# Kernel optimization log

Hardware: AMD Instinct MI355X
Metric: run time of the kernel (lower is better)

The kernel has to match this reference:

```python
import jax, jax.numpy as jnp
import numpy as np

BN_EPS = 1e-5
SEQ_LEN = 256
LSTM_IN = 32
HIDDEN = 512


def setup_inputs() -> dict:
    key = jax.random.key(0)
    ks = jax.random.split(key, 8)
    B, IN_DIM, OUT_DIM = 2048, SEQ_LEN * LSTM_IN, 1
    s_in = 1.0 / np.sqrt(IN_DIM)
    s_h = 1.0 / np.sqrt(HIDDEN)
    return {
        "x": jax.random.normal(ks[0], (B, IN_DIM), jnp.float32),
        "bn_gamma": jnp.ones((IN_DIM,), jnp.float32),
        "bn_beta": jnp.zeros((IN_DIM,), jnp.float32),
        "W_in": jax.random.normal(ks[1], (IN_DIM, IN_DIM), jnp.float32) * s_in,
        "b_in": jax.random.normal(ks[2], (IN_DIM,), jnp.float32) * s_in,
        "W_ih": jax.random.normal(ks[3], (4 * HIDDEN, LSTM_IN), jnp.float32) * s_h,
        "W_hh": jax.random.normal(ks[4], (4 * HIDDEN, HIDDEN), jnp.float32) * s_h,
        "b_ih": jax.random.normal(ks[5], (4 * HIDDEN,), jnp.float32) * s_h,
        "b_hh": jax.random.normal(ks[6], (4 * HIDDEN,), jnp.float32) * s_h,
        "W_out": jax.random.normal(ks[7], (1, HIDDEN), jnp.float32) * s_h,
    }


def reference(x, bn_gamma, bn_beta, W_in, b_in, W_ih, W_hh, b_ih, b_hh, W_out):
    B = x.shape[0]
    # BatchNorm1d (training mode: biased batch statistics)
    mean = jnp.mean(x, axis=0)
    var = jnp.mean((x - mean) ** 2, axis=0)
    out = (x - mean) * jax.lax.rsqrt(var + BN_EPS) * bn_gamma + bn_beta
    # layer_in: Linear(in_dim, in_dim)
    out = out @ W_in.T + b_in
    # split contiguous feature axis into timesteps: [B, T*D] -> [T, B, D]
    xs = out.reshape(B, SEQ_LEN, LSTM_IN).transpose(1, 0, 2)
    # precompute input-to-hidden gates for all steps: [T, B, 4H]
    gates_x = jnp.einsum('tbd,gd->tbg', xs, W_ih) + b_ih + b_hh

    def step(carry, gx):
        h, c = carry
        gates = gx + h @ W_hh.T
        i, f, g, o = jnp.split(gates, 4, axis=-1)
        i = jax.nn.sigmoid(i)
        f = jax.nn.sigmoid(f)
        g = jnp.tanh(g)
        o = jax.nn.sigmoid(o)
        c = f * c + i * g
        h = o * jnp.tanh(c)
        return (h, c), None

    h0 = jnp.zeros((B, HIDDEN), x.dtype)
    c0 = jnp.zeros((B, HIDDEN), x.dtype)
    (h_t, _), _ = jax.lax.scan(step, (h0, c0), gates_x)
    # layer_out: Linear(hidden, out_dim, bias=False)
    return h_t @ W_out.T
```

## Files before the change

### kernel.cpp

```cpp
#include <hip/hip_runtime.h>

#define SEQ   256
#define DIN   8192
#define BATCH 2048
#define HID   512
#define G4    2048
#define KG    544

typedef __attribute__((ext_vector_type(8))) short short8;
typedef __attribute__((ext_vector_type(4))) float f32x4;

static __device__ __forceinline__ unsigned short f2bf(float f) {
  unsigned int u = __float_as_uint(f);
  return (unsigned short)((u + 0x7FFFu + ((u >> 16) & 1u)) >> 16);
}
static __device__ __forceinline__ float bf2f(unsigned short u) {
  return __uint_as_float(((unsigned int)u) << 16);
}
static __device__ __forceinline__ float sigmoidf_(float x) {
  return 1.f / (1.f + __expf(-x));
}
static __device__ __forceinline__ float tanhf_(float x) {
  return 1.f - 2.f / (__expf(2.f * x) + 1.f);
}

__global__ __launch_bounds__(256) void bn_partial(const float* __restrict__ x,
                                                  float* __restrict__ psum,
                                                  float* __restrict__ psq) {
  int c = blockIdx.x * 256 + threadIdx.x;
  int r0 = blockIdx.y * 256;
  float s = 0.f, q = 0.f;
#pragma unroll 8
  for (int r = r0; r < r0 + 256; ++r) {
    float v = x[(size_t)r * DIN + c];
    s += v; q += v * v;
  }
  psum[blockIdx.y * DIN + c] = s;
  psq[blockIdx.y * DIN + c] = q;
}

__global__ __launch_bounds__(256) void bn_finalize(const float* __restrict__ psum,
                                                   const float* __restrict__ psq,
                                                   const float* __restrict__ gamma,
                                                   const float* __restrict__ beta,
                                                   float* __restrict__ scale,
                                                   float* __restrict__ shift) {
  int c = blockIdx.x * 256 + threadIdx.x;
  float s = 0.f, q = 0.f;
#pragma unroll
  for (int i = 0; i < 8; ++i) { s += psum[i * DIN + c]; q += psq[i * DIN + c]; }
  float mean = s * (1.f / BATCH);
  float var = q * (1.f / BATCH) - mean * mean;
  float sc = gamma[c] * rsqrtf(var + 1e-5f);
  scale[c] = sc;
  shift[c] = beta[c] - mean * sc;
}

__global__ __launch_bounds__(256) void cvt_bf16(const float* __restrict__ in,
                                                unsigned short* __restrict__ out, long n) {
  long i = ((long)blockIdx.x * 256 + threadIdx.x) * 8;
  if (i >= n) return;
  float4 a = *(const float4*)(in + i);
  float4 b = *(const float4*)(in + i + 4);
  ushort4 lo, hi;
  lo.x = f2bf(a.x); lo.y = f2bf(a.y); lo.z = f2bf(a.z); lo.w = f2bf(a.w);
  hi.x = f2bf(b.x); hi.y = f2bf(b.y); hi.z = f2bf(b.z); hi.w = f2bf(b.w);
  *(ushort4*)(out + i) = lo;
  *(ushort4*)(out + i + 4) = hi;
}

__global__ __launch_bounds__(256) void build_wg2(const float* __restrict__ W_hh,
                                                 const float* __restrict__ W_ih,
                                                 const float* __restrict__ b_ih,
                                                 const float* __restrict__ b_hh,
                                                 unsigned short* __restrict__ Wg2,
                                                 float* __restrict__ bias2) {
  int gp = blockIdx.x;
  int u = gp >> 2, gate = gp & 3;
  int g = gate * HID + u;
  for (int k = threadIdx.x; k < KG; k += 256) {
    float v = (k < HID) ? W_hh[(size_t)g * HID + k] : W_ih[(size_t)g * 32 + (k - HID)];
    Wg2[(size_t)gp * KG + k] = f2bf(v);
  }
  if (threadIdx.x == 0) bias2[gp] = b_ih[g] + b_hh[g];
}

template<int BF16B>
__global__ __launch_bounds__(256) void gemm1(const float* __restrict__ x,
                                             const float* __restrict__ scale,
                                             const float* __restrict__ shift,
                                             const void* __restrict__ Bsrc,
                                             const float* __restrict__ b_in,
                                             unsigned short* __restrict__ xs) {
  __shared__ unsigned short As[128 * 40];
  __shared__ unsigned short Bs[128 * 40];
  const int tid = threadIdx.x;
  const int lane = tid & 63;
  const int wave = tid >> 6;
  const int wm = (wave >> 1) * 64, wn = (wave & 1) * 64;
  const int bn = blockIdx.x * 128, bm = blockIdx.y * 128;
  const int lr = lane & 15;
  const int kq = (lane >> 4) * 8;

  f32x4 acc[4][4] = {};

  for (int k0 = 0; k0 < DIN; k0 += 32) {
#pragma unroll
    for (int i = 0; i < 4; ++i) {
      int idx = tid + i * 256;
      int row = idx >> 3, c4 = (idx & 7) * 4;
      float4 v = *(const float4*)&x[(size_t)(bm + row) * DIN + k0 + c4];
      float4 sc = *(const float4*)&scale[k0 + c4];
      float4 sh = *(const float4*)&shift[k0 + c4];
      ushort4 o;
      o.x = f2bf(v.x * sc.x + sh.x);
      o.y = f2bf(v.y * sc.y + sh.y);
      o.z = f2bf(v.z * sc.z + sh.z);
      o.w = f2bf(v.w * sc.w + sh.w);
      *(ushort4*)&As[row * 40 + c4] = o;
    }
    if constexpr (BF16B) {
      const unsigned short* W = (const unsigned short*)Bsrc;
#pragma unroll
      for (int i = 0; i < 2; ++i) {
        int idx = tid + i * 256;
        int row = idx >> 2, cc = (idx & 3) * 8;
        *(int4*)&Bs[row * 40 + cc] = *(const int4*)&W[(size_t)(bn + row) * DIN + k0 + cc];
      }
    } else {
      const float* W = (const float*)Bsrc;
#pragma unroll
      for (int i = 0; i < 4; ++i) {
        int idx = tid + i * 256;
        int row = idx >> 3, c4 = (idx & 7) * 4;
        float4 v = *(const float4*)&W[(size_t)(bn + row) * DIN + k0 + c4];
        ushort4 o;
        o.x = f2bf(v.x); o.y = f2bf(v.y); o.z = f2bf(v.z); o.w = f2bf(v.w);
        *(ushort4*)&Bs[row * 40 + c4] = o;
      }
    }
    __syncthreads();
    short8 af[4], bfr[4];
#pragma unroll
    for (int i = 0; i < 4; ++i) af[i] = *(const short8*)&As[(wm + i * 16 + lr) * 40 + kq];
#pragma unroll
    for (int j = 0; j < 4; ++j) bfr[j] = *(const short8*)&Bs[(wn + j * 16 + lr) * 40 + kq];
#pragma unroll
    for (int i = 0; i < 4; ++i)
#pragma unroll
      for (int j = 0; j < 4; ++j)
        acc[i][j] = __builtin_amdgcn_mfma_f32_16x16x32_bf16(af[i], bfr[j], acc[i][j], 0, 0, 0);
    __syncthreads();
  }
#pragma unroll
  for (int i = 0; i < 4; ++i)
#pragma unroll
    for (int j = 0; j < 4; ++j)
#pragma unroll
      for (int r = 0; r < 4; ++r) {
        int row = bm + wm + i * 16 + (lane >> 4) * 4 + r;
        int col = bn + wn + j * 16 + lr;
        float val = acc[i][j][r] + b_in[col];
        xs[((size_t)(col >> 5) * BATCH + row) * 32 + (col & 31)] = f2bf(val);
      }
}

__global__ __launch_bounds__(256) void step_fused(const unsigned short* __restrict__ hin,
                                                  const unsigned short* __restrict__ xst,
                                                  const unsigned short* __restrict__ Wg2,
                                                  const float* __restrict__ bias2,
                                                  float* __restrict__ c,
                                                  unsigned short* __restrict__ hout) {
  __shared__ unsigned short As[64 * 40];
  __shared__ unsigned short Bs[64 * 40];
  __shared__ float gt[64 * 68];
  const int tid = threadIdx.x;
  const int lane = tid & 63;
  const int wave = tid >> 6;
  const int wm = (wave >> 1) * 32, wn = (wave & 1) * 32;
  const int orig = blockIdx.x;
  const int wgid = (orig & 7) * 128 + (orig >> 3);
  const int bx = wgid & 31, by = wgid >> 5;
  const int bm = by * 64, bn = bx * 64;
  const int lr = lane & 15;
  const int kq = (lane >> 4) * 8;
  const int srow = tid >> 2, scc = (tid & 3) * 8;

  f32x4 acc[2][2] = {};

  for (int kt = 0; kt < 17; ++kt) {
    const int k0 = kt * 32;
    int4 av, bv;
    if (kt < 16) av = *(const int4*)&hin[(size_t)(bm + srow) * HID + k0 + scc];
    else         av = *(const int4*)&xst[(size_t)(bm + srow) * 32 + scc];
    bv = *(const int4*)&Wg2[(size_t)(bn + srow) * KG + k0 + scc];
    *(int4*)&As[srow * 40 + scc] = av;
    *(int4*)&Bs[srow * 40 + scc] = bv;
    __syncthreads();
    short8 af[2], bfr[2];
#pragma unroll
    for (int i = 0; i < 2; ++i) af[i] = *(const short8*)&As[(wm + i * 16 + lr) * 40 + kq];
#pragma unroll
    for (int j = 0; j < 2; ++j) bfr[j] = *(const short8*)&Bs[(wn + j * 16 + lr) * 40 + kq];
#pragma unroll
    for (int i = 0; i < 2; ++i)
#pragma unroll
      for (int j = 0; j < 2; ++j)
        acc[i][j] = __builtin_amdgcn_mfma_f32_16x16x32_bf16(af[i], bfr[j], acc[i][j], 0, 0, 0);
    __syncthreads();
  }

#pragma unroll
  for (int i = 0; i < 2; ++i)
#pragma unroll
    for (int j = 0; j < 2; ++j) {
      int colb = wn + j * 16 + lr;
      float bsum = bias2[bn + colb];
#pragma unroll
      for (int r = 0; r < 4; ++r) {
        int row = wm + i * 16 + (lane >> 4) * 4 + r;
        gt[row * 68 + colb] = acc[i][j][r] + bsum;
      }
    }
  __syncthreads();

  {
    const int row = tid >> 2, q = tid & 3;
    const int b = bm + row;
    const int u0 = (bn >> 2) + q * 4;
    const float* gtr = &gt[row * 68 + q * 16];
    const size_t cidx = (size_t)b * HID + u0;
    float4 cold = *(const float4*)&c[cidx];
    float cn[4];
    ushort4 hv;
    const float* co = &cold.x;
#pragma unroll
    for (int k = 0; k < 4; ++k) {
      float iv = sigmoidf_(gtr[k * 4 + 0]);
      float fv = sigmoidf_(gtr[k * 4 + 1]);
      float gv = tanhf_(gtr[k * 4 + 2]);
      float ov = sigmoidf_(gtr[k * 4 + 3]);
      float ccn = fv * co[k] + iv * gv;
      cn[k] = ccn;
      ((unsigned short*)&hv)[k] = f2bf(ov * tanhf_(ccn));
    }
    float4 cw; cw.x = cn[0]; cw.y = cn[1]; cw.z = cn[2]; cw.w = cn[3];
    *(float4*)&c[cidx] = cw;
    *(ushort4*)&hout[cidx] = hv;
  }
}

__global__ __launch_bounds__(64) void gemv_out(const unsigned short* __restrict__ h,
                                               const float* __restrict__ Wout,
                                               float* __restrict__ out) {
  int b = blockIdx.x;
  int lane = threadIdx.x;
  float s = 0.f;
#pragma unroll
  for (int i = 0; i < 8; ++i) {
    int u = lane + i * 64;
    s += bf2f(h[(size_t)b * HID + u]) * Wout[u];
  }
#pragma unroll
  for (int off = 32; off > 0; off >>= 1) s += __shfl_down(s, off);
  if (lane == 0) out[b] = s;
}

extern "C" void kernel_launch(void* const* d_in, const int* in_sizes, int n_in,
                              void* d_out, int out_size, void* d_ws, size_t ws_size,
                              hipStream_t stream) {
  const float* x     = (const float*)d_in[0];
  const float* gamma = (const float*)d_in[1];
  const float* beta  = (const float*)d_in[2];
  const float* W_in  = (const float*)d_in[3];
  const float* b_in  = (const float*)d_in[4];
  const float* W_ih  = (const float*)d_in[5];
  const float* W_hh  = (const float*)d_in[6];
  const float* b_ih  = (const float*)d_in[7];
  const float* b_hh  = (const float*)d_in[8];
  const float* W_out = (const float*)d_in[9];
  float* out = (float*)d_out;

  char* ws = (char*)d_ws;
  float* scale = (float*)(ws + 0);
  float* shift = (float*)(ws + 32768);
  float* bias2 = (float*)(ws + 65536);
  unsigned short* Wg2 = (unsigned short*)(ws + 73728);
  unsigned short* h0  = (unsigned short*)(ws + 2301952);
  unsigned short* h1  = (unsigned short*)(ws + 4399104);
  float* cbuf = (float*)(ws + 6496256);
  unsigned short* xs  = (unsigned short*)(ws + 10690560);
  float* psum = (float*)(ws + 44244992);
  float* psq  = psum + 8 * DIN;
  unsigned short* WinB = (unsigned short*)(ws + 44769280);
  const bool useWinB = ws_size >= (44769280ull + 134217728ull);

  hipMemsetAsync(h0, 0, (size_t)BATCH * HID * 2, stream);
  hipMemsetAsync(cbuf, 0, (size_t)BATCH * HID * 4, stream);

  bn_partial<<<dim3(32, 8), 256, 0, stream>>>(x, psum, psq);
  bn_finalize<<<32, 256, 0, stream>>>(psum, psq, gamma, beta, scale, shift);
  build_wg2<<<G4, 256, 0, stream>>>(W_hh, W_ih, b_ih, b_hh, Wg2, bias2);

  if (useWinB) {
    cvt_bf16<<<32768, 256, 0, stream>>>(W_in, WinB, (long)DIN * DIN);
    gemm1<1><<<dim3(64, 16), 256, 0, stream>>>(x, scale, shift, WinB, b_in, xs);
  } else {
    gemm1<0><<<dim3(64, 16), 256, 0, stream>>>(x, scale, shift, W_in, b_in, xs);
  }

  for (int t = 0; t < SEQ; ++t) {
    const unsigned short* hin = (t & 1) ? h1 : h0;
    unsigned short* hout      = (t & 1) ? h0 : h1;
    step_fused<<<1024, 256, 0, stream>>>(hin, xs + (size_t)t * BATCH * 32, Wg2, bias2, cbuf, hout);
  }
  gemv_out<<<BATCH, 64, 0, stream>>>(h0, W_out, out);
}
```

Measured before the change: 4.039 ms.

## Enlarge LSTM step tiles to 128x128 with register prefetch of next K slice

Measured after the change: 4.868 ms. +20.5%, slower.

```diff
diff --git a/kernel.cpp b/kernel.cpp
--- a/kernel.cpp
+++ b/kernel.cpp
@@ -86,12 +86,12 @@
 }
 
 template<int BF16B>
-__global__ __launch_bounds__(256) void gemm1(const float* __restrict__ x,
-                                             const float* __restrict__ scale,
-                                             const float* __restrict__ shift,
-                                             const void* __restrict__ Bsrc,
-                                             const float* __restrict__ b_in,
-                                             unsigned short* __restrict__ xs) {
+__global__ __launch_bounds__(256) void gemm1_old(const float* __restrict__ x,
+                                                 const float* __restrict__ scale,
+                                                 const float* __restrict__ shift,
+                                                 const void* __restrict__ Bsrc,
+                                                 const float* __restrict__ b_in,
+                                                 unsigned short* __restrict__ xs) {
   __shared__ unsigned short As[128 * 40];
   __shared__ unsigned short Bs[128 * 40];
   const int tid = threadIdx.x;
@@ -165,88 +165,109 @@
       }
 }
 
-__global__ __launch_bounds__(256) void step_fused(const unsigned short* __restrict__ hin,
-                                                  const unsigned short* __restrict__ xst,
-                                                  const unsigned short* __restrict__ Wg2,
-                                                  const float* __restrict__ bias2,
-                                                  float* __restrict__ c,
-                                                  unsigned short* __restrict__ hout) {
-  __shared__ unsigned short As[64 * 40];
-  __shared__ unsigned short Bs[64 * 40];
-  __shared__ float gt[64 * 68];
-  const int tid = threadIdx.x;
-  const int lane = tid & 63;
-  const int wave = tid >> 6;
-  const int wm = (wave >> 1) * 32, wn = (wave & 1) * 32;
-  const int orig = blockIdx.x;
-  const int wgid = (orig & 7) * 128 + (orig >> 3);
-  const int bx = wgid & 31, by = wgid >> 5;
-  const int bm = by * 64, bn = bx * 64;
-  const int lr = lane & 15;
-  const int kq = (lane >> 4) * 8;
+__global__ __launch_bounds__(256) void step_fused4(const unsigned short* __restrict__ hin,
+                                                   const unsigned short* __restrict__ xst,
+                                                   const unsigned short* __restrict__ Wg2,
+                                                   const float* __restrict__ bias2,
+                                                   float* __restrict__ c,
+                                                   unsigned short* __restrict__ hout) {
+  __shared__ unsigned short As[128 * 40];
+  __shared__ unsigned short Bs[128 * 40];
+  __shared__ float gt[64 * 132];
+  const int tid = threadIdx.x, lane = tid & 63, wave = tid >> 6;
+  const int bid = blockIdx.x;
+  const int i4 = bid >> 3;
+  const int bn = ((bid & 7) * 2 + (i4 & 1)) * 128;
+  const int bm = (i4 >> 1) * 128;
+  const int wm = (wave >> 1) * 64, wn = (wave & 1) * 64;
+  const int lr = lane & 15, kq = (lane >> 4) * 8;
   const int srow = tid >> 2, scc = (tid & 3) * 8;
 
-  f32x4 acc[2][2] = {};
+  f32x4 acc[4][4] = {};
+
+  int4 a0 = *(const int4*)&hin[(size_t)(bm + srow) * HID + scc];
+  int4 a1 = *(const int4*)&hin[(size_t)(bm + 64 + srow) * HID + scc];
+  int4 b0 = *(const int4*)&Wg2[(size_t)(bn + srow) * KG + scc];
+  int4 b1 = *(const int4*)&Wg2[(size_t)(bn + 64 + srow) * KG + scc];
 
   for (int kt = 0; kt < 17; ++kt) {
-    const int k0 = kt * 32;
-    int4 av, bv;
-    if (kt < 16) av = *(const int4*)&hin[(size_t)(bm + srow) * HID + k0 + scc];
-    else         av = *(const int4*)&xst[(size_t)(bm + srow) * 32 + scc];
-    bv = *(const int4*)&Wg2[(size_t)(bn + srow) * KG + k0 + scc];
-    *(int4*)&As[srow * 40 + scc] = av;
-    *(int4*)&Bs[srow * 40 + scc] = bv;
-    __syncthreads();
-    short8 af[2], bfr[2];
-#pragma unroll
-    for (int i = 0; i < 2; ++i) af[i] = *(const short8*)&As[(wm + i * 16 + lr) * 40 + kq];
-#pragma unroll
-    for (int j = 0; j < 2; ++j) bfr[j] = *(const short8*)&Bs[(wn + j * 16 + lr) * 40 + kq];
-#pragma unroll
-    for (int i = 0; i < 2; ++i)
-#pragma unroll
-      for (int j = 0; j < 2; ++j)
-        acc[i][j] = __builtin_amdgcn_mfma_f32_16x16x32_bf16(af[i], bfr[j], acc[i][j], 0, 0, 0);
-    __syncthreads();
-  }
-
-#pragma unroll
-  for (int i = 0; i < 2; ++i)
-#pragma unroll
-    for (int j = 0; j < 2; ++j) {
-      int colb = wn + j * 16 + lr;
-      float bsum = bias2[bn + colb];
-#pragma unroll
-      for (int r = 0; r < 4; ++r) {
-        int row = wm + i * 16 + (lane >> 4) * 4 + r;
-        gt[row * 68 + colb] = acc[i][j][r] + bsum;
-      }
-    }
-  __syncthreads();
-
-  {
-    const int row = tid >> 2, q = tid & 3;
-    const int b = bm + row;
-    const int u0 = (bn >> 2) + q * 4;
-    const float* gtr = &gt[row * 68 + q * 16];
-    const size_t cidx = (size_t)b * HID + u0;
-    float4 cold = *(const float4*)&c[cidx];
-    float cn[4];
-    ushort4 hv;
-    const float* co = &cold.x;
-#pragma unroll
-    for (int k = 0; k < 4; ++k) {
-      float iv = sigmoidf_(gtr[k * 4 + 0]);
-      float fv = sigmoidf_(gtr[k * 4 + 1]);
-      float gv = tanhf_(gtr[k * 4 + 2]);
-      float ov = sigmoidf_(gtr[k * 4 + 3]);
-      float ccn = fv * co[k] + iv * gv;
-      cn[k] = ccn;
-      ((unsigned short*)&hv)[k] = f2bf(ov * tanhf_(ccn));
-    }
-    float4 cw; cw.x = cn[0]; cw.y = cn[1]; cw.z = cn[2]; cw.w = cn[3];
-    *(float4*)&c[cidx] = cw;
-    *(ushort4*)&hout[cidx] = hv;
+    __syncthreads();
+    *(int4*)&As[srow * 40 + scc] = a0;
+    *(int4*)&As[(64 + srow) * 40 + scc] = a1;
+    *(int4*)&Bs[srow * 40 + scc] = b0;
+    *(int4*)&Bs[(64 + srow) * 40 + scc] = b1;
+    __syncthreads();
+    if (kt < 16) {
+      const int k1 = (kt + 1) * 32;
+      if (k1 < HID) {
+        a0 = *(const int4*)&hin[(size_t)(bm + srow) * HID + k1 + scc];
+        a1 = *(const int4*)&hin[(size_t)(bm + 64 + srow) * HID + k1 + scc];
+      } else {
+        a0 = *(const int4*)&xst[(size_t)(bm + srow) * 32 + scc];
+        a1 = *(const int4*)&xst[(size_t)(bm + 64 + srow) * 32 + scc];
+      }
+      b0 = *(const int4*)&Wg2[(size_t)(bn + srow) * KG + k1 + scc];
+      b1 = *(const int4*)&Wg2[(size_t)(bn + 64 + srow) * KG + k1 + scc];
+    }
+    short8 af[4], bv[4];
+#pragma unroll
+    for (int a2 = 0; a2 < 4; ++a2) af[a2] = *(const short8*)&As[(wm + a2 * 16 + lr) * 40 + kq];
+#pragma unroll
+    for (int b2 = 0; b2 < 4; ++b2) bv[b2] = *(const short8*)&Bs[(wn + b2 * 16 + lr) * 40 + kq];
+#pragma unroll
+    for (int a2 = 0; a2 < 4; ++a2)
+#pragma unroll
+      for (int b2 = 0; b2 < 4; ++b2)
+        acc[a2][b2] = __builtin_amdgcn_mfma_f32_16x16x32_bf16(af[a2], bv[b2], acc[a2][b2], 0, 0, 0);
+  }
+
+#pragma unroll
+  for (int half = 0; half < 2; ++half) {
+    __syncthreads();
+    if ((wm >> 6) == half) {
+#pragma unroll
+      for (int a2 = 0; a2 < 4; ++a2)
+#pragma unroll
+        for (int b2 = 0; b2 < 2; ++b2) {
+        }
+#pragma unroll
+      for (int a2 = 0; a2 < 4; ++a2)
+#pragma unroll
+        for (int b2 = 0; b2 < 4; ++b2) {
+          const int colb = wn + b2 * 16 + lr;
+          const float bsum = bias2[bn + colb];
+          const int lrow0 = a2 * 16 + (lane >> 4) * 4;
+#pragma unroll
+          for (int r = 0; r < 4; ++r)
+            gt[(lrow0 + r) * 132 + colb] = acc[a2][b2][r] + bsum;
+        }
+    }
+    __syncthreads();
+#pragma unroll
+    for (int p = 0; p < 2; ++p) {
+      const int lrow = p * 32 + (tid >> 3), q = tid & 7;
+      const float* g = &gt[lrow * 132 + q * 16];
+      const size_t cidx = (size_t)(bm + half * 64 + lrow) * HID + (bn >> 2) + q * 4;
+      float4 cold = *(const float4*)&c[cidx];
+      const float* co2 = &cold.x;
+      float cn[4];
+      ushort4 hv;
+#pragma unroll
+      for (int k = 0; k < 4; ++k) {
+        float4 gk = *(const float4*)(g + k * 4);
+        float iv = sigmoidf_(gk.x);
+        float fv = sigmoidf_(gk.y);
+        float gv = tanhf_(gk.z);
+        float ov = sigmoidf_(gk.w);
+        float ccn = fv * co2[k] + iv * gv;
+        cn[k] = ccn;
+        ((unsigned short*)&hv)[k] = f2bf(ov * tanhf_(ccn));
+      }
+      float4 cw;
+      cw.x = cn[0]; cw.y = cn[1]; cw.z = cn[2]; cw.w = cn[3];
+      *(float4*)&c[cidx] = cw;
+      *(ushort4*)&hout[cidx] = hv;
+    }
   }
 }
 
@@ -304,15 +325,15 @@
 
   if (useWinB) {
     cvt_bf16<<<32768, 256, 0, stream>>>(W_in, WinB, (long)DIN * DIN);
-    gemm1<1><<<dim3(64, 16), 256, 0, stream>>>(x, scale, shift, WinB, b_in, xs);
+    gemm1_old<1><<<dim3(64, 16), 256, 0, stream>>>(x, scale, shift, WinB, b_in, xs);
   } else {
-    gemm1<0><<<dim3(64, 16), 256, 0, stream>>>(x, scale, shift, W_in, b_in, xs);
+    gemm1_old<0><<<dim3(64, 16), 256, 0, stream>>>(x, scale, shift, W_in, b_in, xs);
   }
 
   for (int t = 0; t < SEQ; ++t) {
     const unsigned short* hin = (t & 1) ? h1 : h0;
     unsigned short* hout      = (t & 1) ? h0 : h1;
-    step_fused<<<1024, 256, 0, stream>>>(hin, xs + (size_t)t * BATCH * 32, Wg2, bias2, cbuf, hout);
+    step_fused4<<<256, 256, 0, stream>>>(hin, xs + (size_t)t * BATCH * 32, Wg2, bias2, cbuf, hout);
   }
   gemv_out<<<BATCH, 64, 0, stream>>>(h0, W_out, out);
 }
```
